# Kernel tuning notes

Hardware: AMD Instinct MI355X
Metric: run time of the kernel (lower is better)

The kernel has to match this reference:

```python
import jax, jax.numpy as jnp
import numpy as np

N, Q, P, S, B = 262144, 256, 10, 8, 4096


def setup_inputs() -> dict:
    key = jax.random.key(0)
    k1, k2, k3, k4 = jax.random.split(key, 4)
    x = jax.random.normal(k1, (N, Q), dtype=jnp.float32)
    beta_u = jax.random.normal(k2, (Q, P, S), dtype=jnp.float32)
    beta_z = jax.random.normal(k3, (Q, P, S), dtype=jnp.float32)
    seg_ids = jnp.sort(jax.random.randint(k4, (N,), 0, B, dtype=jnp.int64))
    return {"x": x, "beta_u": beta_u, "beta_z": beta_z, "seg_ids": seg_ids,
            "num_segments": B}


def reference(x, beta_u, beta_z, seg_ids, num_segments):
    # b = sqrt(mean over feature dim of beta_z^2): [1, P, S]
    b = jnp.sqrt(jnp.mean(beta_z ** 2, axis=0, keepdims=True))
    eta = beta_z / b                                   # [Q, P, S]
    # attention logits per instance: [N, P, S]
    _w = jnp.einsum('iq,qps->ips', x, beta_u)
    # scatter_softmax over instances within each bag (dim 0)
    seg_max = jax.ops.segment_max(_w, seg_ids, num_segments=num_segments)
    ex = jnp.exp(_w - seg_max[seg_ids])
    denom = jax.ops.segment_sum(ex, seg_ids, num_segments=num_segments)
    w = ex / denom[seg_ids]                            # [N, P, S]
    t = jnp.einsum('iq,qps->ips', x, eta)              # [N, P, S]
    # weighted bag pooling (segment_add_csr equivalent): [B, P, S]
    z_bag = jax.ops.segment_sum(w * t, seg_ids, num_segments=num_segments)
    mean = jnp.mean(z_bag, axis=0)
    std = jnp.std(z_bag, axis=0, ddof=1)               # torch .std is unbiased
    std = jnp.where(jnp.isnan(std), jnp.float32(1.0), std)
    return b * (z_bag - mean) / std
```

## Files before the change

kernel.cpp:

```cpp
#include <hip/hip_runtime.h>
#include <hip/hip_bf16.h>
#include <math.h>

#define NN 262144
#define QQ 256
#define PS 80
#define BB 4096
#define NSLOT 4
#define RT 64
#define NITER 8
#define A_BYTES 8192
#define B_BYTES 10240
#define STG 18432
#define SMEM_BYTES 36864

typedef _Float16 f16x8 __attribute__((ext_vector_type(8)));
typedef float f32x4  __attribute__((ext_vector_type(4)));
typedef const __attribute__((address_space(1))) unsigned int g_u32;
typedef __attribute__((address_space(3))) unsigned int l_u32;

__device__ inline unsigned short f16b(float f) {
  return __builtin_bit_cast(unsigned short, (_Float16)f);
}
__device__ inline float f16tof(unsigned short u) {
  return (float)__builtin_bit_cast(_Float16, u);
}

__global__ void bprep_k(const float* __restrict__ bu, const float* __restrict__ bz,
                        unsigned short* __restrict__ bSwz) {
  int gid = blockIdx.x * 256 + threadIdx.x;
  if (gid >= 5120) return;
  int kt  = gid / 640;
  int rem = gid - kt * 640;
  int kg  = rem / 160;
  int c   = rem - kg * 160;
  int csw = c ^ (kg << 2);
  unsigned short* dst = bSwz + (size_t)kt * 5120 + kg * 1280 + csw * 8;
  int kbase = kt * 32 + kg * 8;
#pragma unroll
  for (int j = 0; j < 8; ++j) {
    int k = kbase + j;
    float v = (c < PS) ? bu[k * PS + c] : bz[k * PS + (c - PS)];
    dst[j] = f16b(v);
  }
}

__global__ void seg_bounds_k(const int* __restrict__ seg, int* __restrict__ segstart) {
  int b = blockIdx.x * blockDim.x + threadIdx.x;
  if (b > BB) return;
  if (b == BB) { segstart[BB] = NN; return; }
  int lo = 0, hi = NN;
  while (lo < hi) {
    int mid = (lo + hi) >> 1;
    if (seg[mid] < b) lo = mid + 1; else hi = mid;
  }
  segstart[b] = lo;
}

__global__ __launch_bounds__(512, 8) void fused_k(
    const float* __restrict__ x, const unsigned short* __restrict__ bSwz,
    const int* __restrict__ seg, const int* __restrict__ segstart,
    float* __restrict__ pm, float* __restrict__ pse, float* __restrict__ pst) {
  __shared__ __align__(16) char smem[SMEM_BYTES];
  const int tid  = threadIdx.x;
  const int wid  = tid >> 6;
  const int lane = tid & 63;
  const int rs   = blockIdx.x * RT;

  const int wr   = (wid & 3) * 16;
  const int cw   = wid >> 2;
  const int lrow = lane & 15;
  const int lk16 = lane >> 4;

  const int ra = tid >> 3;
  const int qa = tid & 7;
  const float* xp = x + (size_t)(rs + ra) * QQ + qa * 4;

  float4 xr[2];

#define BGLOAD(kt_, b_) do {                                                  \
    char* dstb = smem + (b_) * STG + A_BYTES;                                 \
    const char* srcb = (const char*)bSwz + (size_t)(kt_) * B_BYTES;           \
    __builtin_amdgcn_global_load_lds(                                         \
        (g_u32*)(srcb + wid * 1024 + lane * 16),                              \
        (l_u32*)(dstb + wid * 1024), 16, 0, 0);                               \
    if (wid < 2)                                                              \
      __builtin_amdgcn_global_load_lds(                                       \
          (g_u32*)(srcb + 8192 + wid * 1024 + lane * 16),                     \
          (l_u32*)(dstb + 8192 + wid * 1024), 16, 0, 0);                      \
  } while (0)

#define LOADI(s_, t_) do { xr[s_] = *reinterpret_cast<const float4*>(xp + (t_) * 32); } while (0)

#define WRITEI(s_, b_) do {                                                   \
    char* A_ = smem + (b_) * STG;                                             \
    float4 v = xr[s_];                                                        \
    unsigned short h0 = f16b(v.x), h1 = f16b(v.y), h2 = f16b(v.z), h3 = f16b(v.w); \
    unsigned short l0 = f16b(v.x - f16tof(h0)), l1 = f16b(v.y - f16tof(h1));  \
    unsigned short l2 = f16b(v.z - f16tof(h2)), l3 = f16b(v.w - f16tof(h3));  \
    uint2 hw = make_uint2((unsigned)h0 | ((unsigned)h1 << 16),                \
                          (unsigned)h2 | ((unsigned)h3 << 16));               \
    uint2 lw = make_uint2((unsigned)l0 | ((unsigned)l1 << 16),                \
                          (unsigned)l2 | ((unsigned)l3 << 16));               \
    int kg  = qa >> 1;                                                        \
    int rof = (ra ^ (kg << 2)) * 16 + (qa & 1) * 8;                           \
    *reinterpret_cast<uint2*>(A_ + kg * 2048 + rof) = hw;                     \
    *reinterpret_cast<uint2*>(A_ + kg * 2048 + 1024 + rof) = lw;              \
  } while (0)

  f32x4 acc[5];
#pragma unroll
  for (int n = 0; n < 5; ++n) acc[n] = (f32x4){0.f, 0.f, 0.f, 0.f};

  LOADI(0, 0);
  BGLOAD(0, 0);
  WRITEI(0, 0);
  LOADI(1, 1);
  __syncthreads();

#pragma unroll
  for (int t = 0; t < NITER; ++t) {
    if (t < NITER - 1) BGLOAD(t + 1, (t + 1) & 1);
    if (t < NITER - 2) LOADI(t & 1, t + 2);

    const char* A_ = smem + (t & 1) * STG;
    const char* B_ = A_ + A_BYTES;
    int r    = wr + lrow;
    int arof = (r ^ (lk16 << 2)) * 16;
    f16x8 ah = *reinterpret_cast<const f16x8*>(A_ + lk16 * 2048 + arof);
    f16x8 al = *reinterpret_cast<const f16x8*>(A_ + lk16 * 2048 + 1024 + arof);
    __builtin_amdgcn_s_setprio(1);
#pragma unroll
    for (int n = 0; n < 5; ++n) {
      int c = cw * 80 + n * 16 + lrow;
      f16x8 bf = *reinterpret_cast<const f16x8*>(B_ + lk16 * 2560 + ((c ^ (lk16 << 2)) * 16));
      acc[n] = __builtin_amdgcn_mfma_f32_16x16x32_f16(ah, bf, acc[n], 0, 0, 0);
      acc[n] = __builtin_amdgcn_mfma_f32_16x16x32_f16(al, bf, acc[n], 0, 0, 0);
    }
    __builtin_amdgcn_s_setprio(0);

    if (t < NITER - 1) WRITEI((t + 1) & 1, (t + 1) & 1);
    __syncthreads();
  }
#undef BGLOAD
#undef LOADI
#undef WRITEI

  float* res_u          = reinterpret_cast<float*>(smem);
  unsigned short* res_v = reinterpret_cast<unsigned short*>(smem + 20480);
#pragma unroll
  for (int n = 0; n < 5; ++n)
#pragma unroll
    for (int rr = 0; rr < 4; ++rr) {
      int row = wr + lk16 * 4 + rr;
      int col = n * 16 + lrow;
      if (cw == 0) res_u[row * 80 + col] = acc[n][rr];
      else         res_v[row * 80 + col] = f16b(acc[n][rr]);
    }
  __syncthreads();

  int b0 = seg[rs];
  int b1 = seg[rs + RT - 1];
  int nu = (b1 - b0 + 1) * PS;
  for (int u = tid; u < nu; u += 512) {
    int bag = b0 + u / PS;
    int c   = u % PS;
    int sb  = segstart[bag];
    int lo  = max(sb, rs) - rs;
    int hi  = min(segstart[bag + 1], rs + RT) - rs;
    float m_ = -3.4e38f, se = 0.f, st = 0.f;
    for (int r = lo; r < hi; ++r) {
      float v  = res_u[r * 80 + c];
      float tv = f16tof(res_v[r * 80 + c]);
      float nm = fmaxf(m_, v);
      float sc = __expf(m_ - nm);
      float ee = __expf(v - nm);
      se = se * sc + ee;
      st = st * sc + ee * tv;
      m_ = nm;
    }
    int slot = blockIdx.x - (sb >> 6);
    size_t p = ((size_t)bag * NSLOT + slot) * PS + c;
    pm[p] = m_; pse[p] = se; pst[p] = st;
  }
}

__global__ __launch_bounds__(256) void combine_k(
    const int* __restrict__ segstart,
    const float* __restrict__ pm, const float* __restrict__ pse,
    const float* __restrict__ pst, float* __restrict__ zb) {
  int i = blockIdx.x * 256 + threadIdx.x;
  if (i >= BB * PS) return;
  int bag = i / PS, c = i % PS;
  int sb = segstart[bag], eb = segstart[bag + 1];
  float z = 0.f;
  if (eb > sb) {
    int ns = ((eb - 1) >> 6) - (sb >> 6) + 1;
    ns = min(ns, NSLOT);
    float m = -3.4e38f, se = 0.f, st = 0.f;
    for (int s = 0; s < ns; ++s) {
      size_t p = ((size_t)bag * NSLOT + s) * PS + c;
      float m2 = pm[p], se2 = pse[p], st2 = pst[p];
      float nm = fmaxf(m, m2);
      float s1 = __expf(m - nm);
      float s2 = __expf(m2 - nm);
      se = se * s1 + se2 * s2;
      st = st * s1 + st2 * s2;
      m = nm;
    }
    z = st / se;
  }
  zb[i] = z;
}

__device__ inline float wave_sum(float v) {
#pragma unroll
  for (int o = 32; o > 0; o >>= 1) v += __shfl_down(v, o, 64);
  return v;
}

__global__ __launch_bounds__(256) void finalize_k(
    const float* __restrict__ bz, float* __restrict__ zb_out) {
  const int c = blockIdx.x;
  const int t = threadIdx.x;

  float bvz = bz[t * PS + c];
  float bsq = bvz * bvz;

  float s = 0.f, ss = 0.f;
  for (int b = t; b < BB; b += 256) {
    float z = zb_out[b * PS + c];
    s += z;
    ss += z * z;
  }

  __shared__ float w0[4], w1[4], w2[4];
  float a0 = wave_sum(bsq);
  float a1 = wave_sum(s);
  float a2 = wave_sum(ss);
  int wid = t >> 6, lane = t & 63;
  if (lane == 0) { w0[wid] = a0; w1[wid] = a1; w2[wid] = a2; }
  __syncthreads();

  __shared__ float sh[3];
  if (t == 0) {
    float B0 = w0[0] + w0[1] + w0[2] + w0[3];
    float S1 = w1[0] + w1[1] + w1[2] + w1[3];
    float S2 = w2[0] + w2[1] + w2[2] + w2[3];
    float bval = sqrtf(B0 / (float)QQ);
    float mean = S1 / (float)BB;
    float var = (S2 - (float)BB * mean * mean) / (float)(BB - 1);
    float sd = sqrtf(fmaxf(var, 0.f));
    if (!(sd > 0.f) || sd != sd) sd = 1.f;
    sh[0] = bval; sh[1] = mean; sh[2] = sd;
  }
  __syncthreads();
  float bval = sh[0], mean = sh[1], sd = sh[2];
  for (int b = t; b < BB; b += 256) {
    zb_out[b * PS + c] = bval * (zb_out[b * PS + c] - mean) / sd;
  }
}

extern "C" void kernel_launch(void* const* d_in, const int* in_sizes, int n_in,
                              void* d_out, int out_size, void* d_ws, size_t ws_size,
                              hipStream_t stream) {
  const float* x   = (const float*)d_in[0];
  const float* bu  = (const float*)d_in[1];
  const float* bz  = (const float*)d_in[2];
  const int*   seg = (const int*)d_in[3];
  float* out = (float*)d_out;

  char* ws = (char*)d_ws;
  int* segstart        = (int*)ws;
  unsigned short* bSwz = (unsigned short*)(ws + 16640);
  size_t pn  = (size_t)BB * NSLOT * PS;
  float* pm  = (float*)(ws + 98560);
  float* pse = pm + pn;
  float* pst = pse + pn;

  bprep_k<<<20, 256, 0, stream>>>(bu, bz, bSwz);
  seg_bounds_k<<<(BB + 1 + 255) / 256, 256, 0, stream>>>(seg, segstart);
  fused_k<<<NN / RT, 512, 0, stream>>>(x, bSwz, seg, segstart, pm, pse, pst);
  combine_k<<<(BB * PS + 255) / 256, 256, 0, stream>>>(segstart, pm, pse, pst, out);
  finalize_k<<<PS, 256, 0, stream>>>(bz, out);
}
```

Baseline: 119.5 us.

## Drop split-fp16 x correction and use 256-thread blocks with 2x5 MFMA tiles

Removes the hi/lo fp16 split of x so each K-step issues one MFMA per tile instead of two, halving A-tile shared memory. It also halves the block to 4 waves, each computing a 32x80 output tile so every B fragment feeds two MFMAs. This lowers MFMA count and LDS traffic per row but loses the extra precision from the residual term, so logits now carry fp16 rounding of x. Per-wave register use also grows with the doubled accumulator tile.

```diff
diff --git a/kernel.cpp b/kernel.cpp
--- a/kernel.cpp
+++ b/kernel.cpp
@@ -9,10 +9,10 @@
 #define NSLOT 4
 #define RT 64
 #define NITER 8
-#define A_BYTES 8192
+#define A_BYTES 4096
 #define B_BYTES 10240
-#define STG 18432
-#define SMEM_BYTES 36864
+#define STG 14336
+#define SMEM_BYTES 30720
 
 typedef _Float16 f16x8 __attribute__((ext_vector_type(8)));
 typedef float f32x4  __attribute__((ext_vector_type(4)));
@@ -57,7 +57,7 @@
   segstart[b] = lo;
 }
 
-__global__ __launch_bounds__(512, 8) void fused_k(
+__global__ __launch_bounds__(256, 4) void fused_k(
     const float* __restrict__ x, const unsigned short* __restrict__ bSwz,
     const int* __restrict__ seg, const int* __restrict__ segstart,
     float* __restrict__ pm, float* __restrict__ pse, float* __restrict__ pst) {
@@ -67,16 +67,16 @@
   const int lane = tid & 63;
   const int rs   = blockIdx.x * RT;
 
-  const int wr   = (wid & 3) * 16;
-  const int cw   = wid >> 2;
+  const int wr   = (wid & 1) * 32;
+  const int cw   = wid >> 1;
   const int lrow = lane & 15;
   const int lk16 = lane >> 4;
 
-  const int ra = tid >> 3;
-  const int qa = tid & 7;
-  const float* xp = x + (size_t)(rs + ra) * QQ + qa * 4;
-
-  float4 xr[2];
+  const int ra = tid >> 2;
+  const int kg = tid & 3;
+  const float* xp = x + (size_t)(rs + ra) * QQ + kg * 8;
+
+  float4 xr[2][2];
 
 #define BGLOAD(kt_, b_) do {                                                  \
     char* dstb = smem + (b_) * STG + A_BYTES;                                 \
@@ -84,33 +84,37 @@
     __builtin_amdgcn_global_load_lds(                                         \
         (g_u32*)(srcb + wid * 1024 + lane * 16),                              \
         (l_u32*)(dstb + wid * 1024), 16, 0, 0);                               \
+    __builtin_amdgcn_global_load_lds(                                         \
+        (g_u32*)(srcb + 4096 + wid * 1024 + lane * 16),                       \
+        (l_u32*)(dstb + 4096 + wid * 1024), 16, 0, 0);                        \
     if (wid < 2)                                                              \
       __builtin_amdgcn_global_load_lds(                                       \
           (g_u32*)(srcb + 8192 + wid * 1024 + lane * 16),                     \
           (l_u32*)(dstb + 8192 + wid * 1024), 16, 0, 0);                      \
   } while (0)
 
-#define LOADI(s_, t_) do { xr[s_] = *reinterpret_cast<const float4*>(xp + (t_) * 32); } while (0)
+#define LOADI(s_, t_) do {                                                    \
+    xr[s_][0] = *reinterpret_cast<const float4*>(xp + (t_) * 32);             \
+    xr[s_][1] = *reinterpret_cast<const float4*>(xp + (t_) * 32 + 4);         \
+  } while (0)
 
 #define WRITEI(s_, b_) do {                                                   \
-    char* A_ = smem + (b_) * STG;                                             \
-    float4 v = xr[s_];                                                        \
-    unsigned short h0 = f16b(v.x), h1 = f16b(v.y), h2 = f16b(v.z), h3 = f16b(v.w); \
-    unsigned short l0 = f16b(v.x - f16tof(h0)), l1 = f16b(v.y - f16tof(h1));  \
-    unsigned short l2 = f16b(v.z - f16tof(h2)), l3 = f16b(v.w - f16tof(h3));  \
-    uint2 hw = make_uint2((unsigned)h0 | ((unsigned)h1 << 16),                \
-                          (unsigned)h2 | ((unsigned)h3 << 16));               \
-    uint2 lw = make_uint2((unsigned)l0 | ((unsigned)l1 << 16),                \
-                          (unsigned)l2 | ((unsigned)l3 << 16));               \
-    int kg  = qa >> 1;                                                        \
-    int rof = (ra ^ (kg << 2)) * 16 + (qa & 1) * 8;                           \
-    *reinterpret_cast<uint2*>(A_ + kg * 2048 + rof) = hw;                     \
-    *reinterpret_cast<uint2*>(A_ + kg * 2048 + 1024 + rof) = lw;              \
+    float4 v0 = xr[s_][0], v1 = xr[s_][1];                                    \
+    unsigned short a0 = f16b(v0.x), a1 = f16b(v0.y), a2 = f16b(v0.z), a3 = f16b(v0.w); \
+    unsigned short a4 = f16b(v1.x), a5 = f16b(v1.y), a6 = f16b(v1.z), a7 = f16b(v1.w); \
+    uint4 w = make_uint4((unsigned)a0 | ((unsigned)a1 << 16),                 \
+                         (unsigned)a2 | ((unsigned)a3 << 16),                 \
+                         (unsigned)a4 | ((unsigned)a5 << 16),                 \
+                         (unsigned)a6 | ((unsigned)a7 << 16));                \
+    *reinterpret_cast<uint4*>(smem + (b_) * STG + kg * 1024 +                 \
+                              ((ra ^ (kg << 2)) * 16)) = w;                   \
   } while (0)
 
-  f32x4 acc[5];
-#pragma unroll
-  for (int n = 0; n < 5; ++n) acc[n] = (f32x4){0.f, 0.f, 0.f, 0.f};
+  f32x4 acc[2][5];
+#pragma unroll
+  for (int m = 0; m < 2; ++m)
+#pragma unroll
+    for (int n = 0; n < 5; ++n) acc[m][n] = (f32x4){0.f, 0.f, 0.f, 0.f};
 
   LOADI(0, 0);
   BGLOAD(0, 0);
@@ -125,17 +129,19 @@
 
     const char* A_ = smem + (t & 1) * STG;
     const char* B_ = A_ + A_BYTES;
-    int r    = wr + lrow;
-    int arof = (r ^ (lk16 << 2)) * 16;
-    f16x8 ah = *reinterpret_cast<const f16x8*>(A_ + lk16 * 2048 + arof);
-    f16x8 al = *reinterpret_cast<const f16x8*>(A_ + lk16 * 2048 + 1024 + arof);
+    f16x8 ah[2];
+#pragma unroll
+    for (int m = 0; m < 2; ++m) {
+      int r = wr + m * 16 + lrow;
+      ah[m] = *reinterpret_cast<const f16x8*>(A_ + lk16 * 1024 + ((r ^ (lk16 << 2)) * 16));
+    }
     __builtin_amdgcn_s_setprio(1);
 #pragma unroll
     for (int n = 0; n < 5; ++n) {
       int c = cw * 80 + n * 16 + lrow;
       f16x8 bf = *reinterpret_cast<const f16x8*>(B_ + lk16 * 2560 + ((c ^ (lk16 << 2)) * 16));
-      acc[n] = __builtin_amdgcn_mfma_f32_16x16x32_f16(ah, bf, acc[n], 0, 0, 0);
-      acc[n] = __builtin_amdgcn_mfma_f32_16x16x32_f16(al, bf, acc[n], 0, 0, 0);
+      acc[0][n] = __builtin_amdgcn_mfma_f32_16x16x32_f16(ah[0], bf, acc[0][n], 0, 0, 0);
+      acc[1][n] = __builtin_amdgcn_mfma_f32_16x16x32_f16(ah[1], bf, acc[1][n], 0, 0, 0);
     }
     __builtin_amdgcn_s_setprio(0);
 
@@ -149,20 +155,22 @@
   float* res_u          = reinterpret_cast<float*>(smem);
   unsigned short* res_v = reinterpret_cast<unsigned short*>(smem + 20480);
 #pragma unroll
-  for (int n = 0; n < 5; ++n)
-#pragma unroll
-    for (int rr = 0; rr < 4; ++rr) {
-      int row = wr + lk16 * 4 + rr;
-      int col = n * 16 + lrow;
-      if (cw == 0) res_u[row * 80 + col] = acc[n][rr];
-      else         res_v[row * 80 + col] = f16b(acc[n][rr]);
-    }
+  for (int m = 0; m < 2; ++m)
+#pragma unroll
+    for (int n = 0; n < 5; ++n)
+#pragma unroll
+      for (int rr = 0; rr < 4; ++rr) {
+        int row = wr + m * 16 + lk16 * 4 + rr;
+        int col = n * 16 + lrow;
+        if (cw == 0) res_u[row * 80 + col] = acc[m][n][rr];
+        else         res_v[row * 80 + col] = f16b(acc[m][n][rr]);
+      }
   __syncthreads();
 
   int b0 = seg[rs];
   int b1 = seg[rs + RT - 1];
   int nu = (b1 - b0 + 1) * PS;
-  for (int u = tid; u < nu; u += 512) {
+  for (int u = tid; u < nu; u += 256) {
     int bag = b0 + u / PS;
     int c   = u % PS;
     int sb  = segstart[bag];
@@ -280,7 +288,7 @@
 
   bprep_k<<<20, 256, 0, stream>>>(bu, bz, bSwz);
   seg_bounds_k<<<(BB + 1 + 255) / 256, 256, 0, stream>>>(seg, segstart);
-  fused_k<<<NN / RT, 512, 0, stream>>>(x, bSwz, seg, segstart, pm, pse, pst);
+  fused_k<<<NN / RT, 256, 0, stream>>>(x, bSwz, seg, segstart, pm, pse, pst);
   combine_k<<<(BB * PS + 255) / 256, 256, 0, stream>>>(segstart, pm, pse, pst, out);
   finalize_k<<<PS, 256, 0, stream>>>(bz, out);
 }
```

After: 105.0 us. 1.14x faster.
